# Kernel optimization log

Hardware: AMD Instinct MI355X
Metric: run time of the kernel (lower is better)

The kernel has to match this reference:

```python
import jax, jax.numpy as jnp
import numpy as np

# Dims from HierarchicalDecoder defaults; NB is the torch batch size, which the
# original code accidentally uses as the LSTM time axis (2D input to nn.LSTM).
Z_DIM, U, COND, HID, OUT, NB = 512, 16, 512, 1024, 16, 512


def _unif(key, shape, scale):
    return jax.random.uniform(key, shape, jnp.float32, -scale, scale)


def setup_inputs() -> dict:
    key = jax.random.key(0)
    ks = jax.random.split(key, 20)
    d = Z_DIM // U            # 32
    sd = 1.0 / np.sqrt(d)
    sc = 1.0 / np.sqrt(COND)
    sh = 1.0 / np.sqrt(HID)
    return {
        "z": jax.random.normal(ks[0], (NB, Z_DIM), jnp.float32),
        "fc0_w": _unif(ks[1], (COND, d), sd), "fc0_b": _unif(ks[2], (COND,), sd),
        "fc1_w": _unif(ks[3], (HID, COND), sc), "fc1_b": _unif(ks[4], (HID,), sc),
        # conductor LSTM (2 layers, input=hidden=COND); b = b_ih + b_hh fused
        "c_wih0": _unif(ks[5], (4 * COND, COND), sc), "c_whh0": _unif(ks[6], (4 * COND, COND), sc), "c_b0": _unif(ks[7], (4 * COND,), sc),
        "c_wih1": _unif(ks[8], (4 * COND, COND), sc), "c_whh1": _unif(ks[9], (4 * COND, COND), sc), "c_b1": _unif(ks[10], (4 * COND,), sc),
        # decoder LSTM (2 layers, input COND->HID then HID->HID)
        "d_wih0": _unif(ks[11], (4 * HID, COND), sh), "d_whh0": _unif(ks[12], (4 * HID, HID), sh), "d_b0": _unif(ks[13], (4 * HID,), sh),
        "d_wih1": _unif(ks[14], (4 * HID, HID), sh), "d_whh1": _unif(ks[15], (4 * HID, HID), sh), "d_b1": _unif(ks[16], (4 * HID,), sh),
        "out_w": _unif(ks[17], (OUT, HID), sh), "out_b": _unif(ks[18], (OUT,), sh),
    }


def _lstm_layer(x, h0, c0, wih, whh, b):
    # x: [U, T, I]; h0, c0: [U, H]. PyTorch gate order: i, f, g, o.
    gx = jnp.einsum('uti,gi->utg', x, wih) + b  # input contribution, hoisted out of scan

    def step(carry, g):
        h, c = carry
        g = g + h @ whh.T
        i, f, gg, o = jnp.split(g, 4, axis=-1)
        c = jax.nn.sigmoid(f) * c + jax.nn.sigmoid(i) * jnp.tanh(gg)
        h = jax.nn.sigmoid(o) * jnp.tanh(c)
        return (h, c), h

    (hT, _), hs = jax.lax.scan(step, (h0, c0), jnp.swapaxes(gx, 0, 1))
    return jnp.swapaxes(hs, 0, 1), hT  # [U, T, H], [U, H]


def _forward(z, fc0_w, fc0_b, fc1_w, fc1_b, c_wih0, c_whh0, c_b0, c_wih1, c_whh1, c_b1,
             d_wih0, d_whh0, d_b0, d_wih1, d_whh1, d_b1, out_w, out_b):
    B = z.shape[0]
    # [U, B, z_dim//U]; the Python loop over U in the original is vectorized as a batch axis.
    x = jnp.swapaxes(z.reshape(B, U, -1), 0, 1)
    x = jnp.tanh(x @ fc0_w.T + fc0_b)  # fc0 -> [U, B, COND]; B is the LSTM time axis
    zC = jnp.zeros((U, COND), x.dtype)
    h0s, hT0 = _lstm_layer(x, zC, zC, c_wih0, c_whh0, c_b0)
    h1s, hT1 = _lstm_layer(h0s, zC, zC, c_wih1, c_whh1, c_b1)
    # fc1 on final conductor hidden of each layer -> decoder initial h; initial c = 0
    hd0 = jnp.tanh(hT0 @ fc1_w.T + fc1_b)
    hd1 = jnp.tanh(hT1 @ fc1_w.T + fc1_b)
    zH = jnp.zeros((U, HID), x.dtype)
    d0s, _ = _lstm_layer(h1s, hd0, zH, d_wih0, d_whh0, d_b0)
    d1s, _ = _lstm_layer(d0s, hd1, zH, d_wih1, d_whh1, d_b1)
    logits = d1s @ out_w.T + out_b                 # [U, B, OUT]
    probs = jax.nn.softmax(logits, axis=1)         # Softmax(dim=0) over the B axis per subsequence
    return jnp.swapaxes(probs, 0, 1).reshape(B, U * OUT)  # torch.cat(outputs, dim=1)


def reference(z, fc0_w, fc0_b, fc1_w, fc1_b, c_wih0, c_whh0, c_b0, c_wih1, c_whh1, c_b1,
              d_wih0, d_whh0, d_b0, d_wih1, d_whh1, d_b1, out_w, out_b):
    return _forward(z, fc0_w, fc0_b, fc1_w, fc1_b, c_wih0, c_whh0, c_b0, c_wih1, c_whh1, c_b1,
                    d_wih0, d_whh0, d_b0, d_wih1, d_whh1, d_b1, out_w, out_b)
```

## Files before the change

kernel.cpp:

```cpp
#include <hip/hip_runtime.h>
#include <hip/hip_bf16.h>
#include <cstdio>


typedef __attribute__((ext_vector_type(8))) short short8;
typedef __attribute__((ext_vector_type(4))) float f32x4;
using bf16 = __hip_bfloat16;

__device__ __forceinline__ float bfraw2f(short s){
  return __uint_as_float(((unsigned)(unsigned short)s) << 16);
}

__device__ __forceinline__ void gbar_arrive(unsigned* cnt){
  asm volatile("s_waitcnt vmcnt(0)" ::: "memory");
  __syncthreads();
  if (threadIdx.x == 0)
    __hip_atomic_fetch_add(&cnt[(blockIdx.x & 15) * 32], 1u,
                           __ATOMIC_RELAXED, __HIP_MEMORY_SCOPE_AGENT);
}
__device__ __forceinline__ void gbar_wait(const unsigned* cnt, unsigned target){
  if (threadIdx.x < 64){
    const int l = threadIdx.x;
    for (;;){
      bool ok = true;
      if (l < 16)
        ok = __hip_atomic_load(&cnt[l * 32], __ATOMIC_RELAXED,
                               __HIP_MEMORY_SCOPE_AGENT) >= target;
      if (__all(ok)) break;
      __builtin_amdgcn_s_sleep(1);
    }
    __builtin_amdgcn_fence(__ATOMIC_ACQUIRE, "agent");
  }
  __syncthreads();
}

template<int N>
__device__ __forceinline__ void ldA(const bf16* base, short8* av){
#pragma unroll
  for (int i = 0; i < N; ++i)
    av[i] = *(const short8*)(base + i * 32);
}

__device__ __forceinline__ void st2_sc1(bf16* p, unsigned v){
  asm volatile("global_store_short %0, %1, off sc0 sc1" :: "v"(p), "v"(v) : "memory");
}

__device__ __forceinline__ void gates_store(const float v[4], float* c_st, int g,
                                            int kg, int j, bf16* hrow, int Hl,
                                            float* hTp)
{
#pragma unroll
  for (int rr = 0; rr < 4; ++rr){
    float a = (g == 2) ? tanhf(v[rr]) : 1.f / (1.f + expf(-v[rr]));
    float x1 = __shfl_xor(a, 1);
    float x2 = __shfl_xor(a, 2);
    float x3 = __shfl_xor(x1, 2);
    float cn = x1 * c_st[rr] + a * x2;
    float hn = x3 * tanhf(cn);
    c_st[rr] = cn;
    if (g == 0){
      int u = kg * 4 + rr;
      bf16 hb = __float2bfloat16(hn);
      unsigned us = *reinterpret_cast<unsigned short*>(&hb);
      st2_sc1(hrow + (size_t)u * Hl + j, us);
      if (hTp) hTp[(size_t)u * Hl + j] = hn;
    }
  }
}

__global__ void k_prep_w(const float* __restrict__ srcA, const float* __restrict__ srcB,
                         int K1, int K2, int H, bf16* __restrict__ dst)
{
  const int row = blockIdx.x;
  const int j = row >> 2, g = row & 3;
  const int Kt = K1 + K2;
  const float* sA = srcA + (size_t)(g * H + j) * K1;
  const float* sB = srcB ? srcB + (size_t)(g * H + j) * K2 : nullptr;
  bf16* d = dst + (size_t)row * Kt;
  for (int k = threadIdx.x; k < Kt; k += blockDim.x)
    d[k] = __float2bfloat16(k < K1 ? sA[k] : sB[k - K1]);
}

__global__ void k_prep_b(const float* __restrict__ src, int H, float* __restrict__ dst){
  int i = blockIdx.x * blockDim.x + threadIdx.x;
  if (i < 4 * H) dst[i] = src[(i & 3) * H + (i >> 2)];
}

__global__ void k_conv_bf(const float* __restrict__ src, bf16* __restrict__ dst, int n){
  int i = blockIdx.x * blockDim.x + threadIdx.x;
  if (i < n) dst[i] = __float2bfloat16(src[i]);
}

__global__ void k_fc0(const float* __restrict__ z, const float* __restrict__ w,
                      const float* __restrict__ b, bf16* __restrict__ x)
{
  const int m = blockIdx.x;
  const int t = m >> 4, u = m & 15;
  const float* zr = z + (size_t)t * 512 + u * 32;
  float zv[32];
#pragma unroll
  for (int k = 0; k < 32; ++k) zv[k] = zr[k];
  for (int n = threadIdx.x; n < 512; n += 256){
    const float* wr = w + n * 32;
    float s = b[n];
#pragma unroll
    for (int k = 0; k < 32; ++k) s += zv[k] * wr[k];
    x[(size_t)m * 512 + n] = __float2bfloat16(tanhf(s));
  }
}

__device__ __forceinline__ void gload16(const void* g, void* lds_wave_base){
  __builtin_amdgcn_global_load_lds((const __attribute__((address_space(1))) void*)g,
                                   (__attribute__((address_space(3))) void*)lds_wave_base,
                                   16, 0, 0);
}

__global__ __launch_bounds__(256) void k_gemm_gx0(const bf16* __restrict__ A,
                                                  const bf16* __restrict__ W,
                                                  const float* __restrict__ bias,
                                                  float* __restrict__ C)
{
  __shared__ bf16 Al[128 * 64];
  __shared__ bf16 Bl[128 * 64];
  const int tid = threadIdx.x, lane = tid & 63, wave = tid >> 6;
  const int bm = blockIdx.x & 63, bn = blockIdx.x >> 6;
  const int wm = wave >> 1, wn = wave & 1;
  const int col = lane & 15, kg = lane >> 4;

  f32x4 acc[4][4];
#pragma unroll
  for (int i = 0; i < 4; ++i)
#pragma unroll
    for (int q = 0; q < 4; ++q) acc[i][q] = f32x4{0.f, 0.f, 0.f, 0.f};

  const int r = tid >> 3, c8 = (tid & 7) * 8;
  for (int k0 = 0; k0 < 512; k0 += 64){
    const bf16* ga = A + (size_t)(bm * 128 + r) * 512 + k0 + c8;
    const bf16* gb = W + (size_t)(bn * 128 + r) * 512 + k0 + c8;
#pragma unroll
    for (int i = 0; i < 4; ++i){
      gload16(ga + (size_t)32 * i * 512, (char*)Al + (size_t)i * 4096 + wave * 1024);
      gload16(gb + (size_t)32 * i * 512, (char*)Bl + (size_t)i * 4096 + wave * 1024);
    }
    __syncthreads();
#pragma unroll
    for (int kb = 0; kb < 2; ++kb){
      short8 af[4], bfr[4];
#pragma unroll
      for (int i = 0; i < 4; ++i)
        af[i] = *(const short8*)&Al[(wm * 64 + i * 16 + col) * 64 + kb * 32 + kg * 8];
#pragma unroll
      for (int i = 0; i < 4; ++i)
        bfr[i] = *(const short8*)&Bl[(wn * 64 + i * 16 + col) * 64 + kb * 32 + kg * 8];
#pragma unroll
      for (int i = 0; i < 4; ++i)
#pragma unroll
        for (int q = 0; q < 4; ++q)
          acc[i][q] = __builtin_amdgcn_mfma_f32_16x16x32_bf16(af[i], bfr[q], acc[i][q], 0, 0, 0);
    }
    __syncthreads();
  }
#pragma unroll
  for (int i = 0; i < 4; ++i)
#pragma unroll
    for (int q = 0; q < 4; ++q){
      int cc = bn * 128 + wn * 64 + q * 16 + col;
      float bv = bias[cc];
#pragma unroll
      for (int rr = 0; rr < 4; ++rr){
        int rrow = bm * 128 + wm * 64 + i * 16 + kg * 4 + rr;
        C[(size_t)rrow * 2048 + cc] = acc[i][q][rr] + bv;
      }
    }
}

__global__ __launch_bounds__(512, 2) void k_cond(
    const bf16* __restrict__ Wc0, const bf16* __restrict__ Wc1,
    const float* __restrict__ bc1, const float* __restrict__ gx0,
    bf16* h0seq, bf16* h1seq, float* hT0, float* hT1, unsigned* cnt)
{
  const int wg = blockIdx.x, tid = threadIdx.x;
  const int lane = tid & 63, wave = tid >> 6;
  const int col = lane & 15, kg = lane >> 4;
  const int r = col;
  const bool L0 = wg < 16;
  __shared__ f32x4 part[4][64];

  int tileIdx, half = 0;
  if (L0) tileIdx = wg * 8 + wave;
  else  { tileIdx = (wg - 16) * 4 + (wave >> 1); half = wave & 1; }
  const int colp = tileIdx * 16 + col;
  const int j = colp >> 2, g = colp & 3;

  short8 breg[16];
  {
    const bf16* W = L0 ? (Wc0 + (size_t)colp * 512)
                       : (Wc1 + (size_t)colp * 1024 + half * 512);
#pragma unroll
    for (int i = 0; i < 16; ++i) breg[i] = *(const short8*)(W + i * 32 + kg * 8);
  }
#pragma unroll
  for (int i = 0; i < 16; ++i) asm volatile("" : "+v"(breg[i]));

  const float bias = L0 ? 0.f : bc1[colp];
  float c_st[4] = {0.f, 0.f, 0.f, 0.f};
  float gxv[4];
  if (L0){
#pragma unroll
    for (int rr = 0; rr < 4; ++rr)
      gxv[rr] = gx0[((size_t)(kg * 4 + rr)) * 2048 + colp];
  }

  for (int tick = 0; tick < 513; ++tick){
    const int t = tick - (L0 ? 0 : 1);
    const bool active = (t >= 0 && t < 512);
    f32x4 acc = {0.f, 0.f, 0.f, 0.f};
    if (active){
      short8 av[16];
      const bf16* base;
      if (L0)             base = h0seq + (size_t)t * 16 * 512 + r * 512 + kg * 8;
      else if (half == 0) base = h0seq + (size_t)(t + 1) * 16 * 512 + r * 512 + kg * 8;
      else                base = h1seq + (size_t)t * 16 * 512 + r * 512 + kg * 8;
      ldA<16>(base, av);
      asm volatile("s_waitcnt vmcnt(0)" ::: "memory");
      __builtin_amdgcn_sched_barrier(0);
#pragma unroll
      for (int i = 0; i < 16; ++i)
        acc = __builtin_amdgcn_mfma_f32_16x16x32_bf16(av[i], breg[i], acc, 0, 0, 0);
      if (!L0 && half == 1) part[wave >> 1][lane] = acc;
    }
    if (!L0) __syncthreads();
    if (active && (L0 || half == 0)){
      float v[4];
      if (L0){
#pragma unroll
        for (int rr = 0; rr < 4; ++rr) v[rr] = acc[rr] + gxv[rr];
      } else {
        f32x4 p2 = part[wave >> 1][lane];
#pragma unroll
        for (int rr = 0; rr < 4; ++rr) v[rr] = acc[rr] + p2[rr] + bias;
      }
      bf16* hrow = (L0 ? h0seq : h1seq) + (size_t)(t + 1) * 16 * 512;
      float* hTp = (t == 511) ? (L0 ? hT0 : hT1) : nullptr;
      gates_store(v, c_st, g, kg, j, hrow, 512, hTp);
    }
    gbar_arrive(cnt);
    if (L0 && tick + 1 < 512){
#pragma unroll
      for (int rr = 0; rr < 4; ++rr)
        gxv[rr] = gx0[((size_t)(tick + 1) * 16 + kg * 4 + rr) * 2048 + colp];
    }
    gbar_wait(cnt, 3u * (tick + 1));
  }
}

__global__ void k_hd(const float* __restrict__ hT0, const float* __restrict__ hT1,
                     const float* __restrict__ w, const float* __restrict__ b,
                     bf16* __restrict__ d0s0, bf16* __restrict__ d1s0)
{
  int gid = blockIdx.x * 256 + threadIdx.x;
  int sel = gid >> 14;
  int u = (gid >> 10) & 15, n = gid & 1023;
  const float* h = (sel ? hT1 : hT0) + u * 512;
  const float* wr = w + (size_t)n * 512;
  float s = b[n];
  for (int k = 0; k < 512; ++k) s += h[k] * wr[k];
  (sel ? d1s0 : d0s0)[(size_t)u * 1024 + n] = __float2bfloat16(tanhf(s));
}

__global__ __launch_bounds__(512, 2) void k_dec(
    const bf16* __restrict__ Wd0, const bf16* __restrict__ Wd1,
    const float* __restrict__ bd0, const float* __restrict__ bd1,
    const bf16* __restrict__ h1seq, bf16* d0seq, bf16* d1seq, unsigned* cnt)
{
  const int wg = blockIdx.x, tid = threadIdx.x;
  const int lane = tid & 63, wave = tid >> 6;
  const int col = lane & 15, kg = lane >> 4, r = col;
  const bool L0 = wg < 128;
  const int grp = wave >> 2, q = wave & 3;
  const int tileIdx = (L0 ? wg : wg - 128) * 2 + grp;
  const int colp = tileIdx * 16 + col;
  const int j = colp >> 2, g = colp & 3;
  __shared__ f32x4 part[2][3][64];

  short8 breg[16];
#pragma unroll
  for (int i = 0; i < 16; ++i) breg[i] = short8{0,0,0,0,0,0,0,0};
  if (L0){
    const bf16* W = Wd0 + (size_t)colp * 1536 + q * 384;
#pragma unroll
    for (int i = 0; i < 12; ++i) breg[i] = *(const short8*)(W + i * 32 + kg * 8);
  } else {
    const bf16* W = Wd1 + (size_t)colp * 2048 + q * 512;
#pragma unroll
    for (int i = 0; i < 16; ++i) breg[i] = *(const short8*)(W + i * 32 + kg * 8);
  }
#pragma unroll
  for (int i = 0; i < 16; ++i) asm volatile("" : "+v"(breg[i]));

  const float bias = L0 ? bd0[colp] : bd1[colp];
  float c_st[4] = {0.f, 0.f, 0.f, 0.f};

  for (int tick = 0; tick < 513; ++tick){
    const int t = tick - (L0 ? 0 : 1);
    const bool active = (t >= 0 && t < 512);
    f32x4 acc = {0.f, 0.f, 0.f, 0.f};
    if (active){
      short8 av[16];
      if (L0){
        const bf16* h1p = h1seq + (size_t)(t + 1) * 16 * 512 + r * 512 + kg * 8;
        const bf16* d0p = d0seq + (size_t)t * 16 * 1024 + r * 1024 + kg * 8;
        if      (q == 0)  ldA<12>(h1p, av);
        else if (q == 1){ ldA<4>(h1p + 384, av); ldA<8>(d0p, av + 4); }
        else if (q == 2)  ldA<12>(d0p + 256, av);
        else              ldA<12>(d0p + 640, av);
      } else {
        const bf16* d0n = d0seq + (size_t)(t + 1) * 16 * 1024 + r * 1024 + kg * 8;
        const bf16* d1c = d1seq + (size_t)t * 16 * 1024 + r * 1024 + kg * 8;
        if      (q == 0) ldA<16>(d0n, av);
        else if (q == 1) ldA<16>(d0n + 512, av);
        else if (q == 2) ldA<16>(d1c, av);
        else             ldA<16>(d1c + 512, av);
      }
      asm volatile("s_waitcnt vmcnt(0)" ::: "memory");
      __builtin_amdgcn_sched_barrier(0);
      if (L0){
#pragma unroll
        for (int i = 0; i < 12; ++i)
          acc = __builtin_amdgcn_mfma_f32_16x16x32_bf16(av[i], breg[i], acc, 0, 0, 0);
      } else {
#pragma unroll
        for (int i = 0; i < 16; ++i)
          acc = __builtin_amdgcn_mfma_f32_16x16x32_bf16(av[i], breg[i], acc, 0, 0, 0);
      }
      if (q != 0) part[grp][q - 1][lane] = acc;
    }
    __syncthreads();
    if (active && q == 0){
      f32x4 p0 = part[grp][0][lane], p1 = part[grp][1][lane], p2 = part[grp][2][lane];
      float v[4];
#pragma unroll
      for (int rr = 0; rr < 4; ++rr) v[rr] = acc[rr] + p0[rr] + p1[rr] + p2[rr] + bias;
      bf16* hrow = (L0 ? d0seq : d1seq) + (size_t)(t + 1) * 16 * 1024;
      gates_store(v, c_st, g, kg, j, hrow, 1024, nullptr);
    }
    gbar_arrive(cnt);
    gbar_wait(cnt, 16u * (tick + 1));
  }
}

__global__ __launch_bounds__(256) void k_logits(const bf16* __restrict__ d1seq,
                                                const bf16* __restrict__ ow,
                                                const float* __restrict__ ob,
                                                float* __restrict__ logits)
{
  const int u = blockIdx.x >> 4, tb = blockIdx.x & 15;
  __shared__ bf16 rows[32][1024];
  const int tid = threadIdx.x;
  for (int idx = tid; idx < 4096; idx += 256){
    int tl = idx >> 7, seg = idx & 127;
    *(short8*)&rows[tl][seg * 8] =
      *(const short8*)(d1seq + ((size_t)(tb * 32 + tl + 1) * 16 + u) * 1024 + seg * 8);
  }
  __syncthreads();
  for (int p = tid; p < 512; p += 256){
    int tl = p >> 4, o = p & 15;
    const bf16* wr = ow + (size_t)o * 1024;
    float s = 0.f;
    for (int k = 0; k < 1024; k += 8){
      short8 av = *(const short8*)&rows[tl][k];
      short8 wv = *(const short8*)(wr + k);
#pragma unroll
      for (int e = 0; e < 8; ++e) s += bfraw2f(av[e]) * bfraw2f(wv[e]);
    }
    logits[((size_t)u * 16 + o) * 512 + tb * 32 + tl] = s + ob[o];
  }
}

__global__ __launch_bounds__(256) void k_softmax(const float* __restrict__ logits,
                                                 float* __restrict__ out)
{
  const int u = blockIdx.x >> 4, o = blockIdx.x & 15;
  const float* L = logits + ((size_t)u * 16 + o) * 512;
  const int tid = threadIdx.x;
  float v0 = L[tid], v1 = L[tid + 256];
  float m = fmaxf(v0, v1);
  for (int d = 1; d < 64; d <<= 1) m = fmaxf(m, __shfl_xor(m, d));
  __shared__ float red[4], red2[4];
  if ((tid & 63) == 0) red[tid >> 6] = m;
  __syncthreads();
  m = fmaxf(fmaxf(red[0], red[1]), fmaxf(red[2], red[3]));
  float e0 = expf(v0 - m), e1 = expf(v1 - m);
  float s = e0 + e1;
  for (int d = 1; d < 64; d <<= 1) s += __shfl_xor(s, d);
  if ((tid & 63) == 0) red2[tid >> 6] = s;
  __syncthreads();
  s = red2[0] + red2[1] + red2[2] + red2[3];
  float inv = 1.f / s;
  out[(size_t)tid * 256 + u * 16 + o] = e0 * inv;
  out[(size_t)(tid + 256) * 256 + u * 16 + o] = e1 * inv;
}

extern "C" void kernel_launch(void* const* d_in, const int* in_sizes, int n_in,
                              void* d_out, int out_size, void* d_ws, size_t ws_size,
                              hipStream_t stream)
{
  const float* z      = (const float*)d_in[0];
  const float* fc0_w  = (const float*)d_in[1];
  const float* fc0_b  = (const float*)d_in[2];
  const float* fc1_w  = (const float*)d_in[3];
  const float* fc1_b  = (const float*)d_in[4];
  const float* c_wih0 = (const float*)d_in[5];
  const float* c_whh0 = (const float*)d_in[6];
  const float* c_b0   = (const float*)d_in[7];
  const float* c_wih1 = (const float*)d_in[8];
  const float* c_whh1 = (const float*)d_in[9];
  const float* c_b1   = (const float*)d_in[10];
  const float* d_wih0 = (const float*)d_in[11];
  const float* d_whh0 = (const float*)d_in[12];
  const float* d_b0   = (const float*)d_in[13];
  const float* d_wih1 = (const float*)d_in[14];
  const float* d_whh1 = (const float*)d_in[15];
  const float* d_b1   = (const float*)d_in[16];
  const float* out_w  = (const float*)d_in[17];
  const float* out_b  = (const float*)d_in[18];

  char* p = (char*)d_ws;
  auto alloc = [&](size_t bytes) -> char* {
    char* r = p; p += (bytes + 255) & ~(size_t)255; return r;
  };
  bf16*  Wgx0p  = (bf16*)alloc(2048ull * 512 * 2);
  bf16*  Wc0p   = (bf16*)alloc(2048ull * 512 * 2);
  bf16*  Wc1p   = (bf16*)alloc(2048ull * 1024 * 2);
  bf16*  Wd0p   = (bf16*)alloc(4096ull * 1536 * 2);
  bf16*  Wd1p   = (bf16*)alloc(4096ull * 2048 * 2);
  float* bc0p   = (float*)alloc(2048 * 4);
  float* bc1p   = (float*)alloc(2048 * 4);
  float* bd0p   = (float*)alloc(4096 * 4);
  float* bd1p   = (float*)alloc(4096 * 4);
  bf16*  outwbf = (bf16*)alloc(16384 * 2);
  bf16*  x      = (bf16*)alloc(8192ull * 512 * 2);
  float* gx0    = (float*)alloc(8192ull * 2048 * 4);
  bf16*  h0seq  = (bf16*)alloc(513ull * 16 * 512 * 2);
  bf16*  h1seq  = (bf16*)alloc(513ull * 16 * 512 * 2);
  bf16*  d0seq  = (bf16*)alloc(513ull * 16 * 1024 * 2);
  bf16*  d1seq  = (bf16*)alloc(513ull * 16 * 1024 * 2);
  float* hT0    = (float*)alloc(16 * 512 * 4);
  float* hT1    = (float*)alloc(16 * 512 * 4);
  float* logits = (float*)alloc(16ull * 16 * 512 * 4);
  unsigned* cntC = (unsigned*)alloc(16 * 32 * 4);
  unsigned* cntD = (unsigned*)alloc(16 * 32 * 4);
  if ((size_t)(p - (char*)d_ws) > ws_size){
    fprintf(stderr, "kernel_launch: ws too small (%zu needed, %zu given)\n",
            (size_t)(p - (char*)d_ws), ws_size);
    return;
  }

  hipMemsetAsync(cntC, 0, 16 * 32 * 4, stream);
  hipMemsetAsync(cntD, 0, 16 * 32 * 4, stream);
  hipMemsetAsync(h0seq, 0, 16 * 512 * 2, stream);
  hipMemsetAsync(h1seq, 0, 16 * 512 * 2, stream);

  k_prep_w<<<2048, 256, 0, stream>>>(c_wih0, nullptr, 512, 0,   512, Wgx0p);
  k_prep_w<<<2048, 256, 0, stream>>>(c_whh0, nullptr, 512, 0,   512, Wc0p);
  k_prep_w<<<2048, 256, 0, stream>>>(c_wih1, c_whh1, 512, 512,  512, Wc1p);
  k_prep_w<<<4096, 256, 0, stream>>>(d_wih0, d_whh0, 512, 1024, 1024, Wd0p);
  k_prep_w<<<4096, 256, 0, stream>>>(d_wih1, d_whh1, 1024, 1024, 1024, Wd1p);
  k_prep_b<<<8,  256, 0, stream>>>(c_b0, 512,  bc0p);
  k_prep_b<<<8,  256, 0, stream>>>(c_b1, 512,  bc1p);
  k_prep_b<<<16, 256, 0, stream>>>(d_b0, 1024, bd0p);
  k_prep_b<<<16, 256, 0, stream>>>(d_b1, 1024, bd1p);
  k_conv_bf<<<64, 256, 0, stream>>>(out_w, outwbf, 16 * 1024);

  k_fc0<<<8192, 256, 0, stream>>>(z, fc0_w, fc0_b, x);
  k_gemm_gx0<<<1024, 256, 0, stream>>>(x, Wgx0p, bc0p, gx0);

  k_cond<<<48, 512, 0, stream>>>(Wc0p, Wc1p, bc1p, gx0, h0seq, h1seq, hT0, hT1, cntC);
  k_hd<<<128, 256, 0, stream>>>(hT0, hT1, fc1_w, fc1_b, d0seq, d1seq);
  k_dec<<<256, 512, 0, stream>>>(Wd0p, Wd1p, bd0p, bd1p, h1seq, d0seq, d1seq, cntD);

  k_logits<<<256, 256, 0, stream>>>(d1seq, outwbf, out_b, logits);
  k_softmax<<<256, 256, 0, stream>>>(logits, (float*)d_out);
}
```

Baseline: 8.449 ms.

## Consolidate LSTM recurrence into fewer workgroups with full-K per wave

Both persistent LSTM kernels are reorganised so that each wave holds the full reduction dimension of its weight columns in registers. This removes the per-step LDS partial-sum exchange and the extra __syncthreads. Conductor layer 0 now computes four tiles per wave and the workgroup count is halved, which cuts the number of participants in the per-step grid barrier. Hidden-state stores are packed into 8-byte dwordx2 writes via lane shuffles. In exchange, each wave carries many more VGPRs of weights and runs a longer serial MFMA chain per step, which could lengthen the critical path of each step.

Measured after the change: 13.39 ms. 1.58x slower.

```diff
diff --git a/kernel.cpp b/kernel.cpp
--- a/kernel.cpp
+++ b/kernel.cpp
@@ -5,25 +5,31 @@
 
 typedef __attribute__((ext_vector_type(8))) short short8;
 typedef __attribute__((ext_vector_type(4))) float f32x4;
+typedef __attribute__((ext_vector_type(2))) unsigned int u32x2;
 using bf16 = __hip_bfloat16;
 
 __device__ __forceinline__ float bfraw2f(short s){
   return __uint_as_float(((unsigned)(unsigned short)s) << 16);
 }
-
-__device__ __forceinline__ void gbar_arrive(unsigned* cnt){
+__device__ __forceinline__ unsigned bfbits(float f){
+  __hip_bfloat16 h = __float2bfloat16(f);
+  return (unsigned)*reinterpret_cast<unsigned short*>(&h);
+}
+
+__device__ __forceinline__ void gbar_arrive(unsigned* cnt, int cidx){
   asm volatile("s_waitcnt vmcnt(0)" ::: "memory");
   __syncthreads();
   if (threadIdx.x == 0)
-    __hip_atomic_fetch_add(&cnt[(blockIdx.x & 15) * 32], 1u,
+    __hip_atomic_fetch_add(&cnt[cidx * 32], 1u,
                            __ATOMIC_RELAXED, __HIP_MEMORY_SCOPE_AGENT);
 }
+template<int NCNT>
 __device__ __forceinline__ void gbar_wait(const unsigned* cnt, unsigned target){
   if (threadIdx.x < 64){
     const int l = threadIdx.x;
     for (;;){
       bool ok = true;
-      if (l < 16)
+      if (l < NCNT)
         ok = __hip_atomic_load(&cnt[l * 32], __ATOMIC_RELAXED,
                                __HIP_MEMORY_SCOPE_AGENT) >= target;
       if (__all(ok)) break;
@@ -41,14 +47,11 @@
     av[i] = *(const short8*)(base + i * 32);
 }
 
-__device__ __forceinline__ void st2_sc1(bf16* p, unsigned v){
-  asm volatile("global_store_short %0, %1, off sc0 sc1" :: "v"(p), "v"(v) : "memory");
-}
-
-__device__ __forceinline__ void gates_store(const float v[4], float* c_st, int g,
-                                            int kg, int j, bf16* hrow, int Hl,
-                                            float* hTp)
-{
+__device__ __forceinline__ void gate_tile(const float v[4], float* c_st,
+                                          int col, int kg, int jb,
+                                          bf16* hrow, int Hl, float* hTrow)
+{
+  const int g = col & 3;
 #pragma unroll
   for (int rr = 0; rr < 4; ++rr){
     float a = (g == 2) ? tanhf(v[rr]) : 1.f / (1.f + expf(-v[rr]));
@@ -58,12 +61,19 @@
     float cn = x1 * c_st[rr] + a * x2;
     float hn = x3 * tanhf(cn);
     c_st[rr] = cn;
-    if (g == 0){
+    float h4 = __shfl_xor(hn, 4), h8 = __shfl_xor(hn, 8), h12 = __shfl_xor(hn, 12);
+    if (col == 0){
       int u = kg * 4 + rr;
-      bf16 hb = __float2bfloat16(hn);
-      unsigned us = *reinterpret_cast<unsigned short*>(&hb);
-      st2_sc1(hrow + (size_t)u * Hl + j, us);
-      if (hTp) hTp[(size_t)u * Hl + j] = hn;
+      u32x2 pk;
+      pk.x = bfbits(hn) | (bfbits(h4) << 16);
+      pk.y = bfbits(h8) | (bfbits(h12) << 16);
+      bf16* p = hrow + (size_t)u * Hl + jb;
+      asm volatile("global_store_dwordx2 %0, %1, off sc0 sc1"
+                   :: "v"(p), "v"(pk) : "memory");
+      if (hTrow){
+        f32x4 hv = {hn, h4, h8, h12};
+        *(f32x4*)(hTrow + (size_t)u * Hl + jb) = hv;
+      }
     }
   }
 }
@@ -174,83 +184,139 @@
     }
 }
 
-__global__ __launch_bounds__(512, 2) void k_cond(
+__global__ __launch_bounds__(256, 1) void k_cond(
     const bf16* __restrict__ Wc0, const bf16* __restrict__ Wc1,
     const float* __restrict__ bc1, const float* __restrict__ gx0,
     bf16* h0seq, bf16* h1seq, float* hT0, float* hT1, unsigned* cnt)
 {
   const int wg = blockIdx.x, tid = threadIdx.x;
   const int lane = tid & 63, wave = tid >> 6;
-  const int col = lane & 15, kg = lane >> 4;
-  const int r = col;
-  const bool L0 = wg < 16;
-  __shared__ f32x4 part[4][64];
-
-  int tileIdx, half = 0;
-  if (L0) tileIdx = wg * 8 + wave;
-  else  { tileIdx = (wg - 16) * 4 + (wave >> 1); half = wave & 1; }
-  const int colp = tileIdx * 16 + col;
-  const int j = colp >> 2, g = colp & 3;
-
-  short8 breg[16];
-  {
-    const bf16* W = L0 ? (Wc0 + (size_t)colp * 512)
-                       : (Wc1 + (size_t)colp * 1024 + half * 512);
-#pragma unroll
-    for (int i = 0; i < 16; ++i) breg[i] = *(const short8*)(W + i * 32 + kg * 8);
-  }
-#pragma unroll
-  for (int i = 0; i < 16; ++i) asm volatile("" : "+v"(breg[i]));
-
-  const float bias = L0 ? 0.f : bc1[colp];
-  float c_st[4] = {0.f, 0.f, 0.f, 0.f};
-  float gxv[4];
-  if (L0){
-#pragma unroll
-    for (int rr = 0; rr < 4; ++rr)
-      gxv[rr] = gx0[((size_t)(kg * 4 + rr)) * 2048 + colp];
-  }
-
-  for (int tick = 0; tick < 513; ++tick){
-    const int t = tick - (L0 ? 0 : 1);
-    const bool active = (t >= 0 && t < 512);
-    f32x4 acc = {0.f, 0.f, 0.f, 0.f};
-    if (active){
-      short8 av[16];
-      const bf16* base;
-      if (L0)             base = h0seq + (size_t)t * 16 * 512 + r * 512 + kg * 8;
-      else if (half == 0) base = h0seq + (size_t)(t + 1) * 16 * 512 + r * 512 + kg * 8;
-      else                base = h1seq + (size_t)t * 16 * 512 + r * 512 + kg * 8;
-      ldA<16>(base, av);
-      asm volatile("s_waitcnt vmcnt(0)" ::: "memory");
-      __builtin_amdgcn_sched_barrier(0);
+  const int col = lane & 15, kg = lane >> 4, r = col;
+  const int cidx = wg & 7;
+
+  if (wg < 8){
+    const int gw = wg * 4 + wave;
+    const int tile0 = gw * 4;
+    int colp[4];
+#pragma unroll
+    for (int p = 0; p < 4; ++p) colp[p] = (tile0 + p) * 16 + col;
+
+    short8 breg[4][16];
+#pragma unroll
+    for (int p = 0; p < 4; ++p)
 #pragma unroll
       for (int i = 0; i < 16; ++i)
-        acc = __builtin_amdgcn_mfma_f32_16x16x32_bf16(av[i], breg[i], acc, 0, 0, 0);
-      if (!L0 && half == 1) part[wave >> 1][lane] = acc;
-    }
-    if (!L0) __syncthreads();
-    if (active && (L0 || half == 0)){
-      float v[4];
-      if (L0){
-#pragma unroll
-        for (int rr = 0; rr < 4; ++rr) v[rr] = acc[rr] + gxv[rr];
-      } else {
-        f32x4 p2 = part[wave >> 1][lane];
-#pragma unroll
-        for (int rr = 0; rr < 4; ++rr) v[rr] = acc[rr] + p2[rr] + bias;
-      }
-      bf16* hrow = (L0 ? h0seq : h1seq) + (size_t)(t + 1) * 16 * 512;
-      float* hTp = (t == 511) ? (L0 ? hT0 : hT1) : nullptr;
-      gates_store(v, c_st, g, kg, j, hrow, 512, hTp);
-    }
-    gbar_arrive(cnt);
-    if (L0 && tick + 1 < 512){
+        breg[p][i] = *(const short8*)(Wc0 + (size_t)colp[p] * 512 + i * 32 + kg * 8);
+#pragma unroll
+    for (int p = 0; p < 4; ++p)
+#pragma unroll
+      for (int i = 0; i < 16; ++i) asm volatile("" : "+v"(breg[p][i]));
+
+    float c_st[4][4];
+#pragma unroll
+    for (int p = 0; p < 4; ++p)
+#pragma unroll
+      for (int rr = 0; rr < 4; ++rr) c_st[p][rr] = 0.f;
+
+    float gxv[4][4];
+#pragma unroll
+    for (int p = 0; p < 4; ++p)
 #pragma unroll
       for (int rr = 0; rr < 4; ++rr)
-        gxv[rr] = gx0[((size_t)(tick + 1) * 16 + kg * 4 + rr) * 2048 + colp];
-    }
-    gbar_wait(cnt, 3u * (tick + 1));
+        gxv[p][rr] = gx0[((size_t)(kg * 4 + rr)) * 2048 + colp[p]];
+
+    for (int tick = 0; tick < 513; ++tick){
+      const int t = tick;
+      const bool active = t < 512;
+      if (active){
+        short8 av[16];
+        ldA<16>(h0seq + (size_t)t * 8192 + r * 512 + kg * 8, av);
+        f32x4 acc[4];
+#pragma unroll
+        for (int p = 0; p < 4; ++p) acc[p] = f32x4{0.f, 0.f, 0.f, 0.f};
+#pragma unroll
+        for (int i = 0; i < 16; ++i)
+#pragma unroll
+          for (int p = 0; p < 4; ++p)
+            acc[p] = __builtin_amdgcn_mfma_f32_16x16x32_bf16(av[i], breg[p][i], acc[p], 0, 0, 0);
+        bf16* hrow = h0seq + (size_t)(t + 1) * 8192;
+        float* hTp = (t == 511) ? hT0 : nullptr;
+#pragma unroll
+        for (int p = 0; p < 4; ++p){
+          float v[4];
+#pragma unroll
+          for (int rr = 0; rr < 4; ++rr) v[rr] = acc[p][rr] + gxv[p][rr];
+          gate_tile(v, c_st[p], col, kg, (tile0 + p) * 4, hrow, 512, hTp);
+        }
+      }
+      gbar_arrive(cnt, cidx);
+      if (active && t + 1 < 512){
+#pragma unroll
+        for (int p = 0; p < 4; ++p)
+#pragma unroll
+          for (int rr = 0; rr < 4; ++rr)
+            gxv[p][rr] = gx0[((size_t)(t + 1) * 16 + kg * 4 + rr) * 2048 + colp[p]];
+      }
+      gbar_wait<8>(cnt, 3u * (tick + 1));
+    }
+  } else {
+    const int gw = (wg - 8) * 4 + wave;
+    const int tile0 = gw * 2;
+    int colp[2];
+#pragma unroll
+    for (int p = 0; p < 2; ++p) colp[p] = (tile0 + p) * 16 + col;
+
+    short8 breg[2][32];
+#pragma unroll
+    for (int p = 0; p < 2; ++p)
+#pragma unroll
+      for (int i = 0; i < 32; ++i)
+        breg[p][i] = *(const short8*)(Wc1 + (size_t)colp[p] * 1024 + i * 32 + kg * 8);
+#pragma unroll
+    for (int p = 0; p < 2; ++p)
+#pragma unroll
+      for (int i = 0; i < 32; ++i) asm volatile("" : "+v"(breg[p][i]));
+
+    float biasv[2] = {bc1[colp[0]], bc1[colp[1]]};
+    float c_st[2][4];
+#pragma unroll
+    for (int p = 0; p < 2; ++p)
+#pragma unroll
+      for (int rr = 0; rr < 4; ++rr) c_st[p][rr] = 0.f;
+
+    for (int tick = 0; tick < 513; ++tick){
+      const int t = tick - 1;
+      const bool active = (t >= 0 && t < 512);
+      if (active){
+        short8 av[32];
+        ldA<16>(h0seq + (size_t)(t + 1) * 8192 + r * 512 + kg * 8, av);
+        ldA<16>(h1seq + (size_t)t * 8192 + r * 512 + kg * 8, av + 16);
+        f32x4 a0[2], a1[2];
+#pragma unroll
+        for (int p = 0; p < 2; ++p){ a0[p] = f32x4{0.f,0.f,0.f,0.f}; a1[p] = f32x4{0.f,0.f,0.f,0.f}; }
+#pragma unroll
+        for (int i = 0; i < 16; ++i)
+#pragma unroll
+          for (int p = 0; p < 2; ++p)
+            a0[p] = __builtin_amdgcn_mfma_f32_16x16x32_bf16(av[i], breg[p][i], a0[p], 0, 0, 0);
+#pragma unroll
+        for (int i = 0; i < 16; ++i)
+#pragma unroll
+          for (int p = 0; p < 2; ++p)
+            a1[p] = __builtin_amdgcn_mfma_f32_16x16x32_bf16(av[16 + i], breg[p][16 + i], a1[p], 0, 0, 0);
+        bf16* hrow = h1seq + (size_t)(t + 1) * 8192;
+        float* hTp = (t == 511) ? hT1 : nullptr;
+#pragma unroll
+        for (int p = 0; p < 2; ++p){
+          float v[4];
+#pragma unroll
+          for (int rr = 0; rr < 4; ++rr) v[rr] = a0[p][rr] + a1[p][rr] + biasv[p];
+          gate_tile(v, c_st[p], col, kg, (tile0 + p) * 4, hrow, 512, hTp);
+        }
+      }
+      gbar_arrive(cnt, cidx);
+      gbar_wait<8>(cnt, 3u * (tick + 1));
+    }
   }
 }
 
@@ -268,7 +334,7 @@
   (sel ? d1s0 : d0s0)[(size_t)u * 1024 + n] = __float2bfloat16(tanhf(s));
 }
 
-__global__ __launch_bounds__(512, 2) void k_dec(
+__global__ __launch_bounds__(256, 1) void k_dec(
     const bf16* __restrict__ Wd0, const bf16* __restrict__ Wd1,
     const float* __restrict__ bd0, const float* __restrict__ bd1,
     const bf16* __restrict__ h1seq, bf16* d0seq, bf16* d1seq, unsigned* cnt)
@@ -276,76 +342,80 @@
   const int wg = blockIdx.x, tid = threadIdx.x;
   const int lane = tid & 63, wave = tid >> 6;
   const int col = lane & 15, kg = lane >> 4, r = col;
-  const bool L0 = wg < 128;
-  const int grp = wave >> 2, q = wave & 3;
-  const int tileIdx = (L0 ? wg : wg - 128) * 2 + grp;
-  const int colp = tileIdx * 16 + col;
-  const int j = colp >> 2, g = colp & 3;
-  __shared__ f32x4 part[2][3][64];
-
-  short8 breg[16];
-#pragma unroll
-  for (int i = 0; i < 16; ++i) breg[i] = short8{0,0,0,0,0,0,0,0};
-  if (L0){
-    const bf16* W = Wd0 + (size_t)colp * 1536 + q * 384;
-#pragma unroll
-    for (int i = 0; i < 12; ++i) breg[i] = *(const short8*)(W + i * 32 + kg * 8);
-  } else {
-    const bf16* W = Wd1 + (size_t)colp * 2048 + q * 512;
-#pragma unroll
-    for (int i = 0; i < 16; ++i) breg[i] = *(const short8*)(W + i * 32 + kg * 8);
-  }
-#pragma unroll
-  for (int i = 0; i < 16; ++i) asm volatile("" : "+v"(breg[i]));
-
+  const bool L0 = wg < 64;
+  const int tile = (L0 ? wg : wg - 64) * 4 + wave;
+  const int colp = tile * 16 + col;
+  const int jb = tile * 4;
+  const int cidx = wg & 15;
   const float bias = L0 ? bd0[colp] : bd1[colp];
   float c_st[4] = {0.f, 0.f, 0.f, 0.f};
 
-  for (int tick = 0; tick < 513; ++tick){
-    const int t = tick - (L0 ? 0 : 1);
-    const bool active = (t >= 0 && t < 512);
-    f32x4 acc = {0.f, 0.f, 0.f, 0.f};
-    if (active){
-      short8 av[16];
-      if (L0){
-        const bf16* h1p = h1seq + (size_t)(t + 1) * 16 * 512 + r * 512 + kg * 8;
-        const bf16* d0p = d0seq + (size_t)t * 16 * 1024 + r * 1024 + kg * 8;
-        if      (q == 0)  ldA<12>(h1p, av);
-        else if (q == 1){ ldA<4>(h1p + 384, av); ldA<8>(d0p, av + 4); }
-        else if (q == 2)  ldA<12>(d0p + 256, av);
-        else              ldA<12>(d0p + 640, av);
-      } else {
-        const bf16* d0n = d0seq + (size_t)(t + 1) * 16 * 1024 + r * 1024 + kg * 8;
-        const bf16* d1c = d1seq + (size_t)t * 16 * 1024 + r * 1024 + kg * 8;
-        if      (q == 0) ldA<16>(d0n, av);
-        else if (q == 1) ldA<16>(d0n + 512, av);
-        else if (q == 2) ldA<16>(d1c, av);
-        else             ldA<16>(d1c + 512, av);
-      }
-      asm volatile("s_waitcnt vmcnt(0)" ::: "memory");
-      __builtin_amdgcn_sched_barrier(0);
-      if (L0){
-#pragma unroll
-        for (int i = 0; i < 12; ++i)
-          acc = __builtin_amdgcn_mfma_f32_16x16x32_bf16(av[i], breg[i], acc, 0, 0, 0);
-      } else {
+  if (L0){
+    short8 breg[48];
+#pragma unroll
+    for (int i = 0; i < 48; ++i)
+      breg[i] = *(const short8*)(Wd0 + (size_t)colp * 1536 + i * 32 + kg * 8);
+#pragma unroll
+    for (int i = 0; i < 48; ++i) asm volatile("" : "+v"(breg[i]));
+
+    for (int tick = 0; tick < 513; ++tick){
+      const int t = tick;
+      const bool active = t < 512;
+      if (active){
+        short8 av[48];
+        ldA<16>(h1seq + (size_t)(t + 1) * 8192 + r * 512 + kg * 8, av);
+        ldA<32>(d0seq + (size_t)t * 16384 + r * 1024 + kg * 8, av + 16);
+        f32x4 acc0 = {0.f,0.f,0.f,0.f}, acc1 = {0.f,0.f,0.f,0.f};
+#pragma unroll
+        for (int i = 0; i < 24; ++i)
+          acc0 = __builtin_amdgcn_mfma_f32_16x16x32_bf16(av[i], breg[i], acc0, 0, 0, 0);
+#pragma unroll
+        for (int i = 24; i < 48; ++i)
+          acc1 = __builtin_amdgcn_mfma_f32_16x16x32_bf16(av[i], breg[i], acc1, 0, 0, 0);
+        float v[4];
+#pragma unroll
+        for (int rr = 0; rr < 4; ++rr) v[rr] = acc0[rr] + acc1[rr] + bias;
+        gate_tile(v, c_st, col, kg, jb, d0seq + (size_t)(t + 1) * 16384, 1024, nullptr);
+      }
+      gbar_arrive(cnt, cidx);
+      gbar_wait<16>(cnt, 8u * (tick + 1));
+    }
+  } else {
+    short8 breg[64];
+#pragma unroll
+    for (int i = 0; i < 64; ++i)
+      breg[i] = *(const short8*)(Wd1 + (size_t)colp * 2048 + i * 32 + kg * 8);
+#pragma unroll
+    for (int i = 0; i < 64; ++i) asm volatile("" : "+v"(breg[i]));
+
+    for (int tick = 0; tick < 513; ++tick){
+      const int t = tick - 1;
+      const bool active = (t >= 0 && t < 512);
+      if (active){
+        short8 av[32];
+        ldA<32>(d0seq + (size_t)(t + 1) * 16384 + r * 1024 + kg * 8, av);
+        f32x4 acc0 = {0.f,0.f,0.f,0.f}, acc1 = {0.f,0.f,0.f,0.f};
 #pragma unroll
         for (int i = 0; i < 16; ++i)
-          acc = __builtin_amdgcn_mfma_f32_16x16x32_bf16(av[i], breg[i], acc, 0, 0, 0);
-      }
-      if (q != 0) part[grp][q - 1][lane] = acc;
-    }
-    __syncthreads();
-    if (active && q == 0){
-      f32x4 p0 = part[grp][0][lane], p1 = part[grp][1][lane], p2 = part[grp][2][lane];
-      float v[4];
-#pragma unroll
-      for (int rr = 0; rr < 4; ++rr) v[rr] = acc[rr] + p0[rr] + p1[rr] + p2[rr] + bias;
-      bf16* hrow = (L0 ? d0seq : d1seq) + (size_t)(t + 1) * 16 * 1024;
-      gates_store(v, c_st, g, kg, j, hrow, 1024, nullptr);
-    }
-    gbar_arrive(cnt);
-    gbar_wait(cnt, 16u * (tick + 1));
+          acc0 = __builtin_amdgcn_mfma_f32_16x16x32_bf16(av[i], breg[i], acc0, 0, 0, 0);
+#pragma unroll
+        for (int i = 16; i < 32; ++i)
+          acc1 = __builtin_amdgcn_mfma_f32_16x16x32_bf16(av[i], breg[i], acc1, 0, 0, 0);
+        ldA<32>(d1seq + (size_t)t * 16384 + r * 1024 + kg * 8, av);
+#pragma unroll
+        for (int i = 0; i < 16; ++i)
+          acc0 = __builtin_amdgcn_mfma_f32_16x16x32_bf16(av[i], breg[32 + i], acc0, 0, 0, 0);
+#pragma unroll
+        for (int i = 16; i < 32; ++i)
+          acc1 = __builtin_amdgcn_mfma_f32_16x16x32_bf16(av[i], breg[32 + i], acc1, 0, 0, 0);
+        float v[4];
+#pragma unroll
+        for (int rr = 0; rr < 4; ++rr) v[rr] = acc0[rr] + acc1[rr] + bias;
+        gate_tile(v, c_st, col, kg, jb, d1seq + (size_t)(t + 1) * 16384, 1024, nullptr);
+      }
+      gbar_arrive(cnt, cidx);
+      gbar_wait<16>(cnt, 8u * (tick + 1));
+    }
   }
 }
 
@@ -475,9 +545,9 @@
   k_fc0<<<8192, 256, 0, stream>>>(z, fc0_w, fc0_b, x);
   k_gemm_gx0<<<1024, 256, 0, stream>>>(x, Wgx0p, bc0p, gx0);
 
-  k_cond<<<48, 512, 0, stream>>>(Wc0p, Wc1p, bc1p, gx0, h0seq, h1seq, hT0, hT1, cntC);
+  k_cond<<<24, 256, 0, stream>>>(Wc0p, Wc1p, bc1p, gx0, h0seq, h1seq, hT0, hT1, cntC);
   k_hd<<<128, 256, 0, stream>>>(hT0, hT1, fc1_w, fc1_b, d0seq, d1seq);
-  k_dec<<<256, 512, 0, stream>>>(Wd0p, Wd1p, bd0p, bd1p, h1seq, d0seq, d1seq, cntD);
+  k_dec<<<128, 256, 0, stream>>>(Wd0p, Wd1p, bd0p, bd1p, h1seq, d0seq, d1seq, cntD);
 
   k_logits<<<256, 256, 0, stream>>>(d1seq, outwbf, out_b, logits);
   k_softmax<<<256, 256, 0, stream>>>(logits, (float*)d_out);
```

## Halve decoder grid, widen per-wave K slices, pack h stores into dwordx2

Applied to the files above, without the earlier changes.

The decoder persistent kernel drops from 256 to 128 workgroups. Each wave now holds more weight registers (24 or 32 short8) and splits K across two waves instead of four, which reduces the LDS partial-sum reduction. The gate update now gathers four hidden units with shuffles and writes them as one packed dwordx2 store instead of four separate short stores. Barrier counters are also regrouped so each arriving group bumps its own counter and the waiters poll a matching number of slots. The aim is a cheaper grid-wide barrier with fewer participants and less per-step store traffic, at the cost of higher register pressure and longer serial MFMA chains per wave.

Result: slower. 10.09 ms (+19.4%).

```diff
diff --git a/kernel.cpp b/kernel.cpp
--- a/kernel.cpp
+++ b/kernel.cpp
@@ -5,25 +5,31 @@
 
 typedef __attribute__((ext_vector_type(8))) short short8;
 typedef __attribute__((ext_vector_type(4))) float f32x4;
+typedef __attribute__((ext_vector_type(2))) unsigned int u32x2;
 using bf16 = __hip_bfloat16;
 
 __device__ __forceinline__ float bfraw2f(short s){
   return __uint_as_float(((unsigned)(unsigned short)s) << 16);
 }
-
-__device__ __forceinline__ void gbar_arrive(unsigned* cnt){
+__device__ __forceinline__ unsigned bfbits(float f){
+  __hip_bfloat16 h = __float2bfloat16(f);
+  return (unsigned)*reinterpret_cast<unsigned short*>(&h);
+}
+
+__device__ __forceinline__ void gbar_arrive(unsigned* cnt, int cidx){
   asm volatile("s_waitcnt vmcnt(0)" ::: "memory");
   __syncthreads();
   if (threadIdx.x == 0)
-    __hip_atomic_fetch_add(&cnt[(blockIdx.x & 15) * 32], 1u,
+    __hip_atomic_fetch_add(&cnt[cidx * 32], 1u,
                            __ATOMIC_RELAXED, __HIP_MEMORY_SCOPE_AGENT);
 }
+template<int NPOLL>
 __device__ __forceinline__ void gbar_wait(const unsigned* cnt, unsigned target){
   if (threadIdx.x < 64){
     const int l = threadIdx.x;
     for (;;){
       bool ok = true;
-      if (l < 16)
+      if (l < NPOLL)
         ok = __hip_atomic_load(&cnt[l * 32], __ATOMIC_RELAXED,
                                __HIP_MEMORY_SCOPE_AGENT) >= target;
       if (__all(ok)) break;
@@ -40,15 +46,16 @@
   for (int i = 0; i < N; ++i)
     av[i] = *(const short8*)(base + i * 32);
 }
-
-__device__ __forceinline__ void st2_sc1(bf16* p, unsigned v){
-  asm volatile("global_store_short %0, %1, off sc0 sc1" :: "v"(p), "v"(v) : "memory");
-}
-
-__device__ __forceinline__ void gates_store(const float v[4], float* c_st, int g,
-                                            int kg, int j, bf16* hrow, int Hl,
-                                            float* hTp)
-{
+__device__ __forceinline__ void vm0(){
+  asm volatile("s_waitcnt vmcnt(0)" ::: "memory");
+  __builtin_amdgcn_sched_barrier(0);
+}
+
+__device__ __forceinline__ void gate_tile(const float v[4], float* c_st,
+                                          int col, int kg, int jb,
+                                          bf16* hrow, int Hl, float* hTrow)
+{
+  const int g = col & 3;
 #pragma unroll
   for (int rr = 0; rr < 4; ++rr){
     float a = (g == 2) ? tanhf(v[rr]) : 1.f / (1.f + expf(-v[rr]));
@@ -58,12 +65,19 @@
     float cn = x1 * c_st[rr] + a * x2;
     float hn = x3 * tanhf(cn);
     c_st[rr] = cn;
-    if (g == 0){
+    float h4 = __shfl_xor(hn, 4), h8 = __shfl_xor(hn, 8), h12 = __shfl_xor(hn, 12);
+    if (col == 0){
       int u = kg * 4 + rr;
-      bf16 hb = __float2bfloat16(hn);
-      unsigned us = *reinterpret_cast<unsigned short*>(&hb);
-      st2_sc1(hrow + (size_t)u * Hl + j, us);
-      if (hTp) hTp[(size_t)u * Hl + j] = hn;
+      u32x2 pk;
+      pk.x = bfbits(hn) | (bfbits(h4) << 16);
+      pk.y = bfbits(h8) | (bfbits(h12) << 16);
+      bf16* p = hrow + (size_t)u * Hl + jb;
+      asm volatile("global_store_dwordx2 %0, %1, off sc0 sc1"
+                   :: "v"(p), "v"(pk) : "memory");
+      if (hTrow){
+        f32x4 hv = {hn, h4, h8, h12};
+        *(f32x4*)(hTrow + (size_t)u * Hl + jb) = hv;
+      }
     }
   }
 }
@@ -184,13 +198,14 @@
   const int col = lane & 15, kg = lane >> 4;
   const int r = col;
   const bool L0 = wg < 16;
+  const int cidx = L0 ? (wg & 1) : (2 + ((wg - 16) & 3));
   __shared__ f32x4 part[4][64];
 
   int tileIdx, half = 0;
   if (L0) tileIdx = wg * 8 + wave;
   else  { tileIdx = (wg - 16) * 4 + (wave >> 1); half = wave & 1; }
   const int colp = tileIdx * 16 + col;
-  const int j = colp >> 2, g = colp & 3;
+  const int jb = tileIdx * 4;
 
   short8 breg[16];
   {
@@ -218,12 +233,11 @@
     if (active){
       short8 av[16];
       const bf16* base;
-      if (L0)             base = h0seq + (size_t)t * 16 * 512 + r * 512 + kg * 8;
-      else if (half == 0) base = h0seq + (size_t)(t + 1) * 16 * 512 + r * 512 + kg * 8;
-      else                base = h1seq + (size_t)t * 16 * 512 + r * 512 + kg * 8;
+      if (L0)             base = h0seq + (size_t)t * 8192 + r * 512 + kg * 8;
+      else if (half == 0) base = h0seq + (size_t)(t + 1) * 8192 + r * 512 + kg * 8;
+      else                base = h1seq + (size_t)t * 8192 + r * 512 + kg * 8;
       ldA<16>(base, av);
-      asm volatile("s_waitcnt vmcnt(0)" ::: "memory");
-      __builtin_amdgcn_sched_barrier(0);
+      vm0();
 #pragma unroll
       for (int i = 0; i < 16; ++i)
         acc = __builtin_amdgcn_mfma_f32_16x16x32_bf16(av[i], breg[i], acc, 0, 0, 0);
@@ -240,17 +254,18 @@
 #pragma unroll
         for (int rr = 0; rr < 4; ++rr) v[rr] = acc[rr] + p2[rr] + bias;
       }
-      bf16* hrow = (L0 ? h0seq : h1seq) + (size_t)(t + 1) * 16 * 512;
+      bf16* hrow = (L0 ? h0seq : h1seq) + (size_t)(t + 1) * 8192;
       float* hTp = (t == 511) ? (L0 ? hT0 : hT1) : nullptr;
-      gates_store(v, c_st, g, kg, j, hrow, 512, hTp);
-    }
-    gbar_arrive(cnt);
+      gate_tile(v, c_st, col, kg, jb, hrow, 512, hTp);
+    }
+    gbar_arrive(cnt, cidx);
     if (L0 && tick + 1 < 512){
 #pragma unroll
       for (int rr = 0; rr < 4; ++rr)
         gxv[rr] = gx0[((size_t)(tick + 1) * 16 + kg * 4 + rr) * 2048 + colp];
     }
-    gbar_wait(cnt, 3u * (tick + 1));
+    if (L0) gbar_wait<2>(cnt, 8u * (tick + 1));
+    else    gbar_wait<6>(cnt, 8u * (tick + 1));
   }
 }
 
@@ -276,76 +291,117 @@
   const int wg = blockIdx.x, tid = threadIdx.x;
   const int lane = tid & 63, wave = tid >> 6;
   const int col = lane & 15, kg = lane >> 4, r = col;
-  const bool L0 = wg < 128;
-  const int grp = wave >> 2, q = wave & 3;
-  const int tileIdx = (L0 ? wg : wg - 128) * 2 + grp;
-  const int colp = tileIdx * 16 + col;
-  const int j = colp >> 2, g = colp & 3;
-  __shared__ f32x4 part[2][3][64];
-
-  short8 breg[16];
-#pragma unroll
-  for (int i = 0; i < 16; ++i) breg[i] = short8{0,0,0,0,0,0,0,0};
-  if (L0){
-    const bf16* W = Wd0 + (size_t)colp * 1536 + q * 384;
-#pragma unroll
-    for (int i = 0; i < 12; ++i) breg[i] = *(const short8*)(W + i * 32 + kg * 8);
-  } else {
-    const bf16* W = Wd1 + (size_t)colp * 2048 + q * 512;
-#pragma unroll
-    for (int i = 0; i < 16; ++i) breg[i] = *(const short8*)(W + i * 32 + kg * 8);
-  }
-#pragma unroll
-  for (int i = 0; i < 16; ++i) asm volatile("" : "+v"(breg[i]));
+  const bool L0 = wg < 64;
+  const int grp = wave >> 1, q = wave & 1;
+  const int tile = (L0 ? wg : wg - 64) * 4 + grp;
+  const int colp = tile * 16 + col;
+  const int jb = tile * 4;
+  const int cidx = (L0 ? 0 : 8) + (wg & 7);
+  __shared__ f32x4 part[4][64];
 
   const float bias = L0 ? bd0[colp] : bd1[colp];
   float c_st[4] = {0.f, 0.f, 0.f, 0.f};
 
-  for (int tick = 0; tick < 513; ++tick){
-    const int t = tick - (L0 ? 0 : 1);
-    const bool active = (t >= 0 && t < 512);
-    f32x4 acc = {0.f, 0.f, 0.f, 0.f};
-    if (active){
-      short8 av[16];
-      if (L0){
-        const bf16* h1p = h1seq + (size_t)(t + 1) * 16 * 512 + r * 512 + kg * 8;
-        const bf16* d0p = d0seq + (size_t)t * 16 * 1024 + r * 1024 + kg * 8;
-        if      (q == 0)  ldA<12>(h1p, av);
-        else if (q == 1){ ldA<4>(h1p + 384, av); ldA<8>(d0p, av + 4); }
-        else if (q == 2)  ldA<12>(d0p + 256, av);
-        else              ldA<12>(d0p + 640, av);
-      } else {
-        const bf16* d0n = d0seq + (size_t)(t + 1) * 16 * 1024 + r * 1024 + kg * 8;
-        const bf16* d1c = d1seq + (size_t)t * 16 * 1024 + r * 1024 + kg * 8;
-        if      (q == 0) ldA<16>(d0n, av);
-        else if (q == 1) ldA<16>(d0n + 512, av);
-        else if (q == 2) ldA<16>(d1c, av);
-        else             ldA<16>(d1c + 512, av);
+  if (L0){
+    short8 breg[24];
+    {
+      const bf16* Wb = Wd0 + (size_t)colp * 1536 + q * 768;
+#pragma unroll
+      for (int i = 0; i < 24; ++i) breg[i] = *(const short8*)(Wb + i * 32 + kg * 8);
+    }
+#pragma unroll
+    for (int i = 0; i < 24; ++i) asm volatile("" : "+v"(breg[i]));
+
+    for (int tick = 0; tick < 513; ++tick){
+      const int t = tick;
+      const bool active = t < 512;
+      if (active){
+        short8 av[16];
+        f32x4 a0 = {0.f,0.f,0.f,0.f}, a1 = {0.f,0.f,0.f,0.f};
+        const bf16* d0p = d0seq + (size_t)t * 16384 + r * 1024 + kg * 8;
+        if (q == 0){
+          ldA<16>(h1seq + (size_t)(t + 1) * 8192 + r * 512 + kg * 8, av);
+          vm0();
+#pragma unroll
+          for (int i = 0; i < 16; ++i)
+            a0 = __builtin_amdgcn_mfma_f32_16x16x32_bf16(av[i], breg[i], a0, 0, 0, 0);
+          ldA<8>(d0p, av);
+          vm0();
+#pragma unroll
+          for (int i = 0; i < 8; ++i)
+            a1 = __builtin_amdgcn_mfma_f32_16x16x32_bf16(av[i], breg[16 + i], a1, 0, 0, 0);
+        } else {
+          ldA<16>(d0p + 256, av);
+          vm0();
+#pragma unroll
+          for (int i = 0; i < 16; ++i)
+            a0 = __builtin_amdgcn_mfma_f32_16x16x32_bf16(av[i], breg[i], a0, 0, 0, 0);
+          ldA<8>(d0p + 768, av);
+          vm0();
+#pragma unroll
+          for (int i = 0; i < 8; ++i)
+            a1 = __builtin_amdgcn_mfma_f32_16x16x32_bf16(av[i], breg[16 + i], a1, 0, 0, 0);
+        }
+        f32x4 acc;
+#pragma unroll
+        for (int e = 0; e < 4; ++e) acc[e] = a0[e] + a1[e];
+        if (q == 1) part[grp][lane] = acc;
+        __syncthreads();
+        if (q == 0){
+          f32x4 p2 = part[grp][lane];
+          float v[4];
+#pragma unroll
+          for (int rr = 0; rr < 4; ++rr) v[rr] = acc[rr] + p2[rr] + bias;
+          gate_tile(v, c_st, col, kg, jb, d0seq + (size_t)(t + 1) * 16384, 1024, nullptr);
+        }
       }
-      asm volatile("s_waitcnt vmcnt(0)" ::: "memory");
-      __builtin_amdgcn_sched_barrier(0);
-      if (L0){
-#pragma unroll
-        for (int i = 0; i < 12; ++i)
-          acc = __builtin_amdgcn_mfma_f32_16x16x32_bf16(av[i], breg[i], acc, 0, 0, 0);
-      } else {
+      gbar_arrive(cnt, cidx);
+      gbar_wait<8>(cnt, 8u * (tick + 1));
+    }
+  } else {
+    short8 breg[32];
+    {
+      const bf16* Wb = Wd1 + (size_t)colp * 2048 + q * 1024;
+#pragma unroll
+      for (int i = 0; i < 32; ++i) breg[i] = *(const short8*)(Wb + i * 32 + kg * 8);
+    }
+#pragma unroll
+    for (int i = 0; i < 32; ++i) asm volatile("" : "+v"(breg[i]));
+
+    for (int tick = 0; tick < 513; ++tick){
+      const int t = tick - 1;
+      const bool active = (t >= 0 && t < 512);
+      if (active){
+        short8 av[16];
+        f32x4 a0 = {0.f,0.f,0.f,0.f}, a1 = {0.f,0.f,0.f,0.f};
+        const bf16* src = q ? (d1seq + (size_t)t * 16384 + r * 1024 + kg * 8)
+                            : (d0seq + (size_t)(t + 1) * 16384 + r * 1024 + kg * 8);
+        ldA<16>(src, av);
+        vm0();
 #pragma unroll
         for (int i = 0; i < 16; ++i)
-          acc = __builtin_amdgcn_mfma_f32_16x16x32_bf16(av[i], breg[i], acc, 0, 0, 0);
+          a0 = __builtin_amdgcn_mfma_f32_16x16x32_bf16(av[i], breg[i], a0, 0, 0, 0);
+        ldA<16>(src + 512, av);
+        vm0();
+#pragma unroll
+        for (int i = 0; i < 16; ++i)
+          a1 = __builtin_amdgcn_mfma_f32_16x16x32_bf16(av[i], breg[16 + i], a1, 0, 0, 0);
+        f32x4 acc;
+#pragma unroll
+        for (int e = 0; e < 4; ++e) acc[e] = a0[e] + a1[e];
+        if (q == 1) part[grp][lane] = acc;
+        __syncthreads();
+        if (q == 0){
+          f32x4 p2 = part[grp][lane];
+          float v[4];
+#pragma unroll
+          for (int rr = 0; rr < 4; ++rr) v[rr] = acc[rr] + p2[rr] + bias;
+          gate_tile(v, c_st, col, kg, jb, d1seq + (size_t)(t + 1) * 16384, 1024, nullptr);
+        }
       }
-      if (q != 0) part[grp][q - 1][lane] = acc;
-    }
-    __syncthreads();
-    if (active && q == 0){
-      f32x4 p0 = part[grp][0][lane], p1 = part[grp][1][lane], p2 = part[grp][2][lane];
-      float v[4];
-#pragma unroll
-      for (int rr = 0; rr < 4; ++rr) v[rr] = acc[rr] + p0[rr] + p1[rr] + p2[rr] + bias;
-      bf16* hrow = (L0 ? d0seq : d1seq) + (size_t)(t + 1) * 16 * 1024;
-      gates_store(v, c_st, g, kg, j, hrow, 1024, nullptr);
-    }
-    gbar_arrive(cnt);
-    gbar_wait(cnt, 16u * (tick + 1));
+      gbar_arrive(cnt, cidx);
+      gbar_wait<16>(cnt, 8u * (tick + 1));
+    }
   }
 }
 
@@ -477,7 +533,7 @@
 
   k_cond<<<48, 512, 0, stream>>>(Wc0p, Wc1p, bc1p, gx0, h0seq, h1seq, hT0, hT1, cntC);
   k_hd<<<128, 256, 0, stream>>>(hT0, hT1, fc1_w, fc1_b, d0seq, d1seq);
-  k_dec<<<256, 512, 0, stream>>>(Wd0p, Wd1p, bd0p, bd1p, h1seq, d0seq, d1seq, cntD);
+  k_dec<<<128, 512, 0, stream>>>(Wd0p, Wd1p, bd0p, bd1p, h1seq, d0seq, d1seq, cntD);
 
   k_logits<<<256, 256, 0, stream>>>(d1seq, outwbf, out_b, logits);
   k_softmax<<<256, 256, 0, stream>>>(logits, (float*)d_out);
```
